# Kernel tuning notes

Hardware: AMD Instinct MI355X
Metric: run time of the kernel (lower is better)

## Reference

```python
import jax, jax.numpy as jnp
import numpy as np

N_NODES = 100000


def gcn_conv(x, W, b, src, dst, n):
    """PyG GCNConv with default add_self_loops and symmetric normalization."""
    xw = x @ W  # [N, out]
    loop = jnp.arange(n, dtype=src.dtype)
    s = jnp.concatenate([src, loop])  # source j
    d = jnp.concatenate([dst, loop])  # target i
    deg = jax.ops.segment_sum(jnp.ones_like(d, dtype=xw.dtype), d, num_segments=n)
    dinv = jnp.where(deg > 0, jax.lax.rsqrt(deg), 0.0)
    norm = dinv[s] * dinv[d]  # [E+N]
    msg = xw[s] * norm[:, None]
    out = jax.ops.segment_sum(msg, d, num_segments=n)
    return out + b


def setup_inputs() -> dict:
    key = jax.random.key(0)
    ks = jax.random.split(key, 9)
    n, e, f = N_NODES, 1600000, 512
    x = jax.random.normal(ks[0], (n, f), dtype=jnp.float32)
    edge_index = jax.random.randint(ks[1], (2, e), 0, n, dtype=jnp.int32)
    y = jax.random.uniform(ks[2], (n, 1), dtype=jnp.float32)
    W1 = jax.random.normal(ks[3], (f, 64), dtype=jnp.float32) / np.sqrt(f)
    b1 = jnp.zeros((64,), jnp.float32)
    W2 = jax.random.normal(ks[4], (64, 256), dtype=jnp.float32) / np.sqrt(64)
    b2 = jnp.zeros((256,), jnp.float32)
    W3 = jax.random.normal(ks[5], (256, 1), dtype=jnp.float32) / np.sqrt(256)
    b3 = jnp.zeros((1,), jnp.float32)
    return {"x": x, "edge_index": edge_index, "y": y,
            "W1": W1, "b1": b1, "W2": W2, "b2": b2, "W3": W3, "b3": b3}


def reference(x, edge_index, y, W1, b1, W2, b2, W3, b3):
    n = x.shape[0]
    src, dst = edge_index[0], edge_index[1]
    h = jax.nn.relu(gcn_conv(x, W1, b1, src, dst, n))
    # dropout is identity in eval mode
    h = jax.nn.relu(gcn_conv(h, W2, b2, src, dst, n))
    z = gcn_conv(h, W3, b3, src, dst, n)  # logits [N, 1]
    # BCE(sigmoid(z), y), computed stably via log-sigmoid
    loss = -(y * jax.nn.log_sigmoid(z) + (1.0 - y) * jax.nn.log_sigmoid(-z))
    return jnp.mean(loss)
```

## Files before the change

### kernel.cpp

```cpp
#include <hip/hip_runtime.h>
#include <math.h>

typedef __attribute__((ext_vector_type(8))) short s16x8;
typedef __attribute__((ext_vector_type(4))) float f32x4;

__device__ inline ushort f2bf(float f) {
    union { float f; unsigned u; } v; v.f = f;
    unsigned r = v.u + 0x7FFF + ((v.u >> 16) & 1);
    return (ushort)(r >> 16);
}
__device__ inline float bf2f(ushort h) {
    union { unsigned u; float f; } v; v.u = ((unsigned)h) << 16;
    return v.f;
}


__global__ void hist_kernel(const int* __restrict__ dst, int E, int* __restrict__ cnt) {
    int e = blockIdx.x * blockDim.x + threadIdx.x;
    if (e < E) atomicAdd(&cnt[dst[e]], 1);
}

__global__ void alloc_kernel(const int* __restrict__ cnt, int* __restrict__ row_start,
                             float* __restrict__ dinv, int* __restrict__ total, int N) {
    int i = blockIdx.x * blockDim.x + threadIdx.x;
    int lane = threadIdx.x & 63;
    int c = (i < N) ? cnt[i] : 0;
    int inc = c;
#pragma unroll
    for (int o = 1; o < 64; o <<= 1) {
        int v = __shfl_up(inc, o, 64);
        if (lane >= o) inc += v;
    }
    int wsum = __shfl(inc, 63, 64);
    int base = 0;
    if (lane == 0) base = atomicAdd(total, wsum);
    base = __shfl(base, 0, 64);
    if (i < N) {
        row_start[i] = base + inc - c;
        dinv[i] = rsqrtf((float)(c + 1));
    }
}

__global__ void scatter_kernel(const int* __restrict__ src, const int* __restrict__ dst, int E,
                               const int* __restrict__ row_start, int* __restrict__ cursor,
                               int* __restrict__ csr) {
    int e = blockIdx.x * blockDim.x + threadIdx.x;
    if (e < E) {
        int d = dst[e];
        int p = row_start[d] + atomicAdd(&cursor[d], 1);
        csr[p] = src[e];
    }
}

__global__ void wsplit_kernel(const float* __restrict__ W, ushort* __restrict__ wt_hi,
                              ushort* __restrict__ wt_lo) {
    int idx = blockIdx.x * blockDim.x + threadIdx.x;
    if (idx < 64 * 512) {
        int n = idx & 63, k = idx >> 6;
        float f = W[k * 64 + n];
        ushort h = f2bf(f);
        wt_hi[n * 512 + k] = h;
        wt_lo[n * 512 + k] = f2bf(f - bf2f(h));
    }
}

__global__ __launch_bounds__(256, 3) void gemm1_kernel(const float* __restrict__ x,
                                                       const ushort* __restrict__ wt_hi,
                                                       const ushort* __restrict__ wt_lo,
                                                       float* __restrict__ out, int N) {
    __shared__ __align__(16) short xs_hi[128 * 64];
    __shared__ __align__(16) short xs_lo[128 * 64];
    __shared__ __align__(16) short ws_hi[64 * 64];
    __shared__ __align__(16) short ws_lo[64 * 64];

    const int tid = threadIdx.x;
    const int nodeBase = blockIdx.x * 128;
    const int wave = tid >> 6, lane = tid & 63;
    const int m16 = lane & 15, quad = lane >> 4;

    f32x4 acc[2][4];
#pragma unroll
    for (int mt = 0; mt < 2; mt++)
#pragma unroll
        for (int nt = 0; nt < 4; nt++) acc[mt][nt] = (f32x4){0.f, 0.f, 0.f, 0.f};

    for (int kc = 0; kc < 512; kc += 64) {
        __syncthreads();
#pragma unroll
        for (int i = 0; i < 4; i++) {
            int f = tid + i * 256;
            int node = f >> 3, g = f & 7;
            int gn = nodeBase + node;
            if (gn >= N) gn = N - 1;
            const float4 a = *(const float4*)(x + (size_t)gn * 512 + kc + g * 8);
            const float4 b = *(const float4*)(x + (size_t)gn * 512 + kc + g * 8 + 4);
            float ff[8] = {a.x, a.y, a.z, a.w, b.x, b.y, b.z, b.w};
            union { ushort u[8]; uint4 v; } H, L;
#pragma unroll
            for (int j = 0; j < 8; j++) {
                ushort h = f2bf(ff[j]);
                H.u[j] = h;
                L.u[j] = f2bf(ff[j] - bf2f(h));
            }
            int gp = (g + node) & 7;
            *(uint4*)&xs_hi[node * 64 + gp * 8] = H.v;
            *(uint4*)&xs_lo[node * 64 + gp * 8] = L.v;
        }
#pragma unroll
        for (int i = 0; i < 2; i++) {
            int f = tid + i * 256;
            int n = f >> 3, g = f & 7;
            int gp = (g + n) & 7;
            *(uint4*)&ws_hi[n * 64 + gp * 8] =
                *(const uint4*)(wt_hi + (size_t)n * 512 + kc + g * 8);
            *(uint4*)&ws_lo[n * 64 + gp * 8] =
                *(const uint4*)(wt_lo + (size_t)n * 512 + kc + g * 8);
        }
        __syncthreads();
#pragma unroll
        for (int ck = 0; ck < 2; ck++) {
            s16x8 Ah[2], Al[2];
#pragma unroll
            for (int mt = 0; mt < 2; mt++) {
                int row = (wave * 2 + mt) * 16 + m16;
                int gp = (ck * 4 + quad + row) & 7;
                Ah[mt] = *(s16x8*)&xs_hi[row * 64 + gp * 8];
                Al[mt] = *(s16x8*)&xs_lo[row * 64 + gp * 8];
            }
#pragma unroll
            for (int nt = 0; nt < 4; nt++) {
                int n = nt * 16 + m16;
                int gp = (ck * 4 + quad + n) & 7;
                s16x8 Bh = *(s16x8*)&ws_hi[n * 64 + gp * 8];
                s16x8 Bl = *(s16x8*)&ws_lo[n * 64 + gp * 8];
#pragma unroll
                for (int mt = 0; mt < 2; mt++) {
                    acc[mt][nt] = __builtin_amdgcn_mfma_f32_16x16x32_bf16(Ah[mt], Bh, acc[mt][nt], 0, 0, 0);
                    acc[mt][nt] = __builtin_amdgcn_mfma_f32_16x16x32_bf16(Ah[mt], Bl, acc[mt][nt], 0, 0, 0);
                    acc[mt][nt] = __builtin_amdgcn_mfma_f32_16x16x32_bf16(Al[mt], Bh, acc[mt][nt], 0, 0, 0);
                }
            }
        }
    }
#pragma unroll
    for (int mt = 0; mt < 2; mt++) {
#pragma unroll
        for (int r = 0; r < 4; r++) {
            int gn = nodeBase + (wave * 2 + mt) * 16 + quad * 4 + r;
            if (gn < N) {
#pragma unroll
                for (int nt = 0; nt < 4; nt++)
                    out[(size_t)gn * 64 + nt * 16 + m16] = acc[mt][nt][r];
            }
        }
    }
}

template <int RELU, int BIAS>
__global__ void agg64_kernel(const float* __restrict__ in, float* __restrict__ out,
                             const int* __restrict__ row_start, const int* __restrict__ cnt,
                             const int* __restrict__ csr, const float* __restrict__ dinv,
                             const float* __restrict__ bias, int N) {
    int gw = (int)((blockIdx.x * (size_t)blockDim.x + threadIdx.x) >> 6);
    int lane = threadIdx.x & 63;
    if (gw >= N) return;
    float di = dinv[gw];
    float acc = di * di * in[(size_t)gw * 64 + lane];
    int s = row_start[gw];
    int c = cnt[gw];
    int e = 0;
    for (; e + 8 <= c; e += 8) {
        int j0 = csr[s + e + 0], j1 = csr[s + e + 1], j2 = csr[s + e + 2], j3 = csr[s + e + 3];
        int j4 = csr[s + e + 4], j5 = csr[s + e + 5], j6 = csr[s + e + 6], j7 = csr[s + e + 7];
        float v0 = in[(size_t)j0 * 64 + lane];
        float v1 = in[(size_t)j1 * 64 + lane];
        float v2 = in[(size_t)j2 * 64 + lane];
        float v3 = in[(size_t)j3 * 64 + lane];
        float v4 = in[(size_t)j4 * 64 + lane];
        float v5 = in[(size_t)j5 * 64 + lane];
        float v6 = in[(size_t)j6 * 64 + lane];
        float v7 = in[(size_t)j7 * 64 + lane];
        float s0 = dinv[j0] * v0 + dinv[j1] * v1 + dinv[j2] * v2 + dinv[j3] * v3;
        float s1 = dinv[j4] * v4 + dinv[j5] * v5 + dinv[j6] * v6 + dinv[j7] * v7;
        acc += di * (s0 + s1);
    }
    for (; e < c; e++) {
        int j = csr[s + e];
        acc += di * dinv[j] * in[(size_t)j * 64 + lane];
    }
    if (BIAS) acc += bias[lane];
    if (RELU) acc = fmaxf(acc, 0.f);
    out[(size_t)gw * 64 + lane] = acc;
}

__global__ __launch_bounds__(256, 2) void gemm23_kernel(const float* __restrict__ a2,
                                                        const float* __restrict__ W2,
                                                        const float* __restrict__ b2,
                                                        const float* __restrict__ W3,
                                                        float* __restrict__ t, int N) {
    __shared__ float w2s[64 * 256];
    __shared__ float b2s[256];
    __shared__ float w3s[256];
    const int tid = threadIdx.x;
#pragma unroll
    for (int i = 0; i < 16; i++) {
        int f4 = tid + i * 256;
        *(float4*)&w2s[f4 * 4] = *(const float4*)&W2[f4 * 4];
    }
    b2s[tid] = b2[tid];
    w3s[tid] = W3[tid];
    __syncthreads();

    const int lane = tid & 63;
    const int wave = tid >> 6;
    const int nodeBase = blockIdx.x * 64 + wave * 16;

    float4 w3f = *(const float4*)&w3s[lane * 4];
    float4 b2f = *(const float4*)&b2s[lane * 4];

    float acc[16][4];
#pragma unroll
    for (int n = 0; n < 16; n++) {
        acc[n][0] = 0.f; acc[n][1] = 0.f; acc[n][2] = 0.f; acc[n][3] = 0.f;
    }

    for (int k4 = 0; k4 < 64; k4 += 4) {
        float4 wf0 = *(const float4*)&w2s[(k4 + 0) * 256 + lane * 4];
        float4 wf1 = *(const float4*)&w2s[(k4 + 1) * 256 + lane * 4];
        float4 wf2 = *(const float4*)&w2s[(k4 + 2) * 256 + lane * 4];
        float4 wf3 = *(const float4*)&w2s[(k4 + 3) * 256 + lane * 4];
#pragma unroll
        for (int n = 0; n < 16; n++) {
            int gn = nodeBase + n;
            if (gn >= N) gn = N - 1;
            float4 av = *(const float4*)&a2[(size_t)gn * 64 + k4];
            acc[n][0] = fmaf(av.x, wf0.x, acc[n][0]);
            acc[n][1] = fmaf(av.x, wf0.y, acc[n][1]);
            acc[n][2] = fmaf(av.x, wf0.z, acc[n][2]);
            acc[n][3] = fmaf(av.x, wf0.w, acc[n][3]);
            acc[n][0] = fmaf(av.y, wf1.x, acc[n][0]);
            acc[n][1] = fmaf(av.y, wf1.y, acc[n][1]);
            acc[n][2] = fmaf(av.y, wf1.z, acc[n][2]);
            acc[n][3] = fmaf(av.y, wf1.w, acc[n][3]);
            acc[n][0] = fmaf(av.z, wf2.x, acc[n][0]);
            acc[n][1] = fmaf(av.z, wf2.y, acc[n][1]);
            acc[n][2] = fmaf(av.z, wf2.z, acc[n][2]);
            acc[n][3] = fmaf(av.z, wf2.w, acc[n][3]);
            acc[n][0] = fmaf(av.w, wf3.x, acc[n][0]);
            acc[n][1] = fmaf(av.w, wf3.y, acc[n][1]);
            acc[n][2] = fmaf(av.w, wf3.z, acc[n][2]);
            acc[n][3] = fmaf(av.w, wf3.w, acc[n][3]);
        }
    }

#pragma unroll
    for (int n = 0; n < 16; n++) {
        float r0 = fmaxf(acc[n][0] + b2f.x, 0.f);
        float r1 = fmaxf(acc[n][1] + b2f.y, 0.f);
        float r2 = fmaxf(acc[n][2] + b2f.z, 0.f);
        float r3 = fmaxf(acc[n][3] + b2f.w, 0.f);
        float p = r0 * w3f.x + r1 * w3f.y + r2 * w3f.z + r3 * w3f.w;
#pragma unroll
        for (int off = 32; off > 0; off >>= 1) p += __shfl_down(p, off, 64);
        int gn = nodeBase + n;
        if (lane == 0 && gn < N) t[gn] = p;
    }
}

__global__ void loss_kernel(const float* __restrict__ t, const float* __restrict__ dinv,
                            const int* __restrict__ row_start, const int* __restrict__ cnt,
                            const int* __restrict__ csr, const float* __restrict__ y,
                            const float* __restrict__ b3, float* __restrict__ out,
                            int N, float invN) {
    int i = blockIdx.x * blockDim.x + threadIdx.x;
    float loss = 0.f;
    if (i < N) {
        float di = dinv[i];
        float aedge = 0.f;
        int s = row_start[i], c = cnt[i];
        int e = 0;
        for (; e + 4 <= c; e += 4) {
            int j0 = csr[s + e + 0], j1 = csr[s + e + 1];
            int j2 = csr[s + e + 2], j3 = csr[s + e + 3];
            aedge += dinv[j0] * t[j0] + dinv[j1] * t[j1] + dinv[j2] * t[j2] + dinv[j3] * t[j3];
        }
        for (; e < c; e++) { int j = csr[s + e]; aedge += dinv[j] * t[j]; }
        float z = di * (di * t[i] + aedge) + b3[0];
        float yv = y[i];
        float L = log1pf(expf(-fabsf(z)));
        float spz  = fmaxf(z, 0.f) + L;
        float spnz = fmaxf(-z, 0.f) + L;
        loss = yv * spnz + (1.f - yv) * spz;
    }
#pragma unroll
    for (int off = 32; off > 0; off >>= 1) loss += __shfl_down(loss, off, 64);
    __shared__ float red[4];
    int lane = threadIdx.x & 63, wave = threadIdx.x >> 6;
    if (lane == 0) red[wave] = loss;
    __syncthreads();
    if (threadIdx.x == 0)
        atomicAdd(out, (red[0] + red[1] + red[2] + red[3]) * invN);
}

extern "C" void kernel_launch(void* const* d_in, const int* in_sizes, int n_in,
                              void* d_out, int out_size, void* d_ws, size_t ws_size,
                              hipStream_t stream) {
    const float* x  = (const float*)d_in[0];
    const int*   ei = (const int*)d_in[1];
    const float* y  = (const float*)d_in[2];
    const float* W1 = (const float*)d_in[3];
    const float* b1 = (const float*)d_in[4];
    const float* W2 = (const float*)d_in[5];
    const float* b2 = (const float*)d_in[6];
    const float* W3 = (const float*)d_in[7];
    const float* b3 = (const float*)d_in[8];

    const int N = in_sizes[2];
    const int E = in_sizes[1] / 2;
    const int* src  = ei;
    const int* dstp = ei + E;

    char* w = (char*)d_ws;
    int*    cnt       = (int*)w;    w += (size_t)N * 4;
    int*    cursor    = (int*)w;    w += (size_t)N * 4;
    int*    total     = (int*)w;    w += 16;
    int*    row_start = (int*)w;    w += (size_t)N * 4;
    float*  dinv      = (float*)w;  w += (size_t)N * 4;
    int*    csr       = (int*)w;    w += (size_t)E * 4;
    ushort* wt_hi     = (ushort*)w; w += (size_t)64 * 512 * 2;
    ushort* wt_lo     = (ushort*)w; w += (size_t)64 * 512 * 2;
    float*  bufA      = (float*)w;  w += (size_t)N * 64 * 4;
    float*  bufB      = (float*)w;  w += (size_t)N * 64 * 4;

    hipMemsetAsync(cnt, 0, (size_t)N * 8 + 16, stream);
    hipMemsetAsync(d_out, 0, sizeof(float), stream);

    const int tb = 256;
    wsplit_kernel<<<(64 * 512 + tb - 1) / tb, tb, 0, stream>>>(W1, wt_hi, wt_lo);
    hist_kernel<<<(E + tb - 1) / tb, tb, 0, stream>>>(dstp, E, cnt);
    alloc_kernel<<<(N + tb - 1) / tb, tb, 0, stream>>>(cnt, row_start, dinv, total, N);
    scatter_kernel<<<(E + tb - 1) / tb, tb, 0, stream>>>(src, dstp, E, row_start, cursor, csr);

    gemm1_kernel<<<(N + 127) / 128, 256, 0, stream>>>(x, wt_hi, wt_lo, bufA, N);
    agg64_kernel<1, 1><<<(N + 3) / 4, 256, 0, stream>>>(bufA, bufB, row_start, cnt, csr, dinv, b1, N);

    agg64_kernel<0, 0><<<(N + 3) / 4, 256, 0, stream>>>(bufB, bufA, row_start, cnt, csr, dinv, nullptr, N);

    gemm23_kernel<<<(N + 63) / 64, 256, 0, stream>>>(bufA, W2, b2, W3, bufB, N);

    loss_kernel<<<(N + tb - 1) / tb, tb, 0, stream>>>(bufB, dinv, row_start, cnt, csr, y, b3,
                                                      (float*)d_out, N, 1.0f / N);
}
```

Baseline: 749.2 us.

## Store intermediate features in bf16 with dinv pre-scaled into source rows

Intermediate node-feature buffers change from fp32 to bf16, which halves the bytes gathered per edge in the two aggregation passes and in the dense layer-2/3 read. The source-side dinv factor is folded into the producer (GEMM1 epilogue, first aggregation, gemm23 output), so gather loops become plain sums without per-neighbour dinv loads. This trades fp32 precision for bf16 rounding of activations, which may shift the loss slightly.

```diff
diff --git a/kernel.cpp b/kernel.cpp
--- a/kernel.cpp
+++ b/kernel.cpp
@@ -12,6 +12,12 @@
 __device__ inline float bf2f(ushort h) {
     union { unsigned u; float f; } v; v.u = ((unsigned)h) << 16;
     return v.f;
+}
+__device__ inline float bfLo(unsigned u) {
+    union { unsigned x; float f; } v; v.x = u << 16; return v.f;
+}
+__device__ inline float bfHi(unsigned u) {
+    union { unsigned x; float f; } v; v.x = u & 0xFFFF0000u; return v.f;
 }
 
 
@@ -67,7 +73,8 @@
 __global__ __launch_bounds__(256, 3) void gemm1_kernel(const float* __restrict__ x,
                                                        const ushort* __restrict__ wt_hi,
                                                        const ushort* __restrict__ wt_lo,
-                                                       float* __restrict__ out, int N) {
+                                                       const float* __restrict__ dinv,
+                                                       ushort* __restrict__ out, int N) {
     __shared__ __align__(16) short xs_hi[128 * 64];
     __shared__ __align__(16) short xs_lo[128 * 64];
     __shared__ __align__(16) short ws_hi[64 * 64];
@@ -148,56 +155,58 @@
         for (int r = 0; r < 4; r++) {
             int gn = nodeBase + (wave * 2 + mt) * 16 + quad * 4 + r;
             if (gn < N) {
+                float di = dinv[gn];
 #pragma unroll
                 for (int nt = 0; nt < 4; nt++)
-                    out[(size_t)gn * 64 + nt * 16 + m16] = acc[mt][nt][r];
+                    out[(size_t)gn * 64 + nt * 16 + m16] = f2bf(di * acc[mt][nt][r]);
             }
         }
     }
 }
 
-template <int RELU, int BIAS>
-__global__ void agg64_kernel(const float* __restrict__ in, float* __restrict__ out,
-                             const int* __restrict__ row_start, const int* __restrict__ cnt,
-                             const int* __restrict__ csr, const float* __restrict__ dinv,
-                             const float* __restrict__ bias, int N) {
+template <int RELU, int BIAS, int PREMUL>
+__global__ void agg64bf_kernel(const ushort* __restrict__ in, ushort* __restrict__ out,
+                               const int* __restrict__ row_start, const int* __restrict__ cnt,
+                               const int* __restrict__ csr, const float* __restrict__ dinv,
+                               const float* __restrict__ bias, int N) {
     int gw = (int)((blockIdx.x * (size_t)blockDim.x + threadIdx.x) >> 6);
     int lane = threadIdx.x & 63;
     if (gw >= N) return;
-    float di = dinv[gw];
-    float acc = di * di * in[(size_t)gw * 64 + lane];
+    float acc = bf2f(in[(size_t)gw * 64 + lane]);
     int s = row_start[gw];
     int c = cnt[gw];
     int e = 0;
     for (; e + 8 <= c; e += 8) {
         int j0 = csr[s + e + 0], j1 = csr[s + e + 1], j2 = csr[s + e + 2], j3 = csr[s + e + 3];
         int j4 = csr[s + e + 4], j5 = csr[s + e + 5], j6 = csr[s + e + 6], j7 = csr[s + e + 7];
-        float v0 = in[(size_t)j0 * 64 + lane];
-        float v1 = in[(size_t)j1 * 64 + lane];
-        float v2 = in[(size_t)j2 * 64 + lane];
-        float v3 = in[(size_t)j3 * 64 + lane];
-        float v4 = in[(size_t)j4 * 64 + lane];
-        float v5 = in[(size_t)j5 * 64 + lane];
-        float v6 = in[(size_t)j6 * 64 + lane];
-        float v7 = in[(size_t)j7 * 64 + lane];
-        float s0 = dinv[j0] * v0 + dinv[j1] * v1 + dinv[j2] * v2 + dinv[j3] * v3;
-        float s1 = dinv[j4] * v4 + dinv[j5] * v5 + dinv[j6] * v6 + dinv[j7] * v7;
-        acc += di * (s0 + s1);
+        float v0 = bf2f(in[(size_t)j0 * 64 + lane]);
+        float v1 = bf2f(in[(size_t)j1 * 64 + lane]);
+        float v2 = bf2f(in[(size_t)j2 * 64 + lane]);
+        float v3 = bf2f(in[(size_t)j3 * 64 + lane]);
+        float v4 = bf2f(in[(size_t)j4 * 64 + lane]);
+        float v5 = bf2f(in[(size_t)j5 * 64 + lane]);
+        float v6 = bf2f(in[(size_t)j6 * 64 + lane]);
+        float v7 = bf2f(in[(size_t)j7 * 64 + lane]);
+        acc += ((v0 + v1) + (v2 + v3)) + ((v4 + v5) + (v6 + v7));
     }
     for (; e < c; e++) {
         int j = csr[s + e];
-        acc += di * dinv[j] * in[(size_t)j * 64 + lane];
-    }
-    if (BIAS) acc += bias[lane];
-    if (RELU) acc = fmaxf(acc, 0.f);
-    out[(size_t)gw * 64 + lane] = acc;
-}
-
-__global__ __launch_bounds__(256, 2) void gemm23_kernel(const float* __restrict__ a2,
+        acc += bf2f(in[(size_t)j * 64 + lane]);
+    }
+    float di = dinv[gw];
+    float v = di * acc;
+    if (BIAS) v += bias[lane];
+    if (RELU) v = fmaxf(v, 0.f);
+    if (PREMUL) v *= di;
+    out[(size_t)gw * 64 + lane] = f2bf(v);
+}
+
+__global__ __launch_bounds__(256, 2) void gemm23_kernel(const ushort* __restrict__ a2,
                                                         const float* __restrict__ W2,
                                                         const float* __restrict__ b2,
                                                         const float* __restrict__ W3,
-                                                        float* __restrict__ t, int N) {
+                                                        const float* __restrict__ dinv,
+                                                        float* __restrict__ r, int N) {
     __shared__ float w2s[64 * 256];
     __shared__ float b2s[256];
     __shared__ float w3s[256];
@@ -233,23 +242,24 @@
         for (int n = 0; n < 16; n++) {
             int gn = nodeBase + n;
             if (gn >= N) gn = N - 1;
-            float4 av = *(const float4*)&a2[(size_t)gn * 64 + k4];
-            acc[n][0] = fmaf(av.x, wf0.x, acc[n][0]);
-            acc[n][1] = fmaf(av.x, wf0.y, acc[n][1]);
-            acc[n][2] = fmaf(av.x, wf0.z, acc[n][2]);
-            acc[n][3] = fmaf(av.x, wf0.w, acc[n][3]);
-            acc[n][0] = fmaf(av.y, wf1.x, acc[n][0]);
-            acc[n][1] = fmaf(av.y, wf1.y, acc[n][1]);
-            acc[n][2] = fmaf(av.y, wf1.z, acc[n][2]);
-            acc[n][3] = fmaf(av.y, wf1.w, acc[n][3]);
-            acc[n][0] = fmaf(av.z, wf2.x, acc[n][0]);
-            acc[n][1] = fmaf(av.z, wf2.y, acc[n][1]);
-            acc[n][2] = fmaf(av.z, wf2.z, acc[n][2]);
-            acc[n][3] = fmaf(av.z, wf2.w, acc[n][3]);
-            acc[n][0] = fmaf(av.w, wf3.x, acc[n][0]);
-            acc[n][1] = fmaf(av.w, wf3.y, acc[n][1]);
-            acc[n][2] = fmaf(av.w, wf3.z, acc[n][2]);
-            acc[n][3] = fmaf(av.w, wf3.w, acc[n][3]);
+            uint2 u = *(const uint2*)(a2 + (size_t)gn * 64 + k4);
+            float a0 = bfLo(u.x), a1 = bfHi(u.x), a2v = bfLo(u.y), a3 = bfHi(u.y);
+            acc[n][0] = fmaf(a0, wf0.x, acc[n][0]);
+            acc[n][1] = fmaf(a0, wf0.y, acc[n][1]);
+            acc[n][2] = fmaf(a0, wf0.z, acc[n][2]);
+            acc[n][3] = fmaf(a0, wf0.w, acc[n][3]);
+            acc[n][0] = fmaf(a1, wf1.x, acc[n][0]);
+            acc[n][1] = fmaf(a1, wf1.y, acc[n][1]);
+            acc[n][2] = fmaf(a1, wf1.z, acc[n][2]);
+            acc[n][3] = fmaf(a1, wf1.w, acc[n][3]);
+            acc[n][0] = fmaf(a2v, wf2.x, acc[n][0]);
+            acc[n][1] = fmaf(a2v, wf2.y, acc[n][1]);
+            acc[n][2] = fmaf(a2v, wf2.z, acc[n][2]);
+            acc[n][3] = fmaf(a2v, wf2.w, acc[n][3]);
+            acc[n][0] = fmaf(a3, wf3.x, acc[n][0]);
+            acc[n][1] = fmaf(a3, wf3.y, acc[n][1]);
+            acc[n][2] = fmaf(a3, wf3.z, acc[n][2]);
+            acc[n][3] = fmaf(a3, wf3.w, acc[n][3]);
         }
     }
 
@@ -263,11 +273,11 @@
 #pragma unroll
         for (int off = 32; off > 0; off >>= 1) p += __shfl_down(p, off, 64);
         int gn = nodeBase + n;
-        if (lane == 0 && gn < N) t[gn] = p;
-    }
-}
-
-__global__ void loss_kernel(const float* __restrict__ t, const float* __restrict__ dinv,
+        if (lane == 0 && gn < N) r[gn] = dinv[gn] * p;
+    }
+}
+
+__global__ void loss_kernel(const float* __restrict__ r, const float* __restrict__ dinv,
                             const int* __restrict__ row_start, const int* __restrict__ cnt,
                             const int* __restrict__ csr, const float* __restrict__ y,
                             const float* __restrict__ b3, float* __restrict__ out,
@@ -275,17 +285,16 @@
     int i = blockIdx.x * blockDim.x + threadIdx.x;
     float loss = 0.f;
     if (i < N) {
-        float di = dinv[i];
-        float aedge = 0.f;
+        float aedge = r[i];
         int s = row_start[i], c = cnt[i];
         int e = 0;
         for (; e + 4 <= c; e += 4) {
             int j0 = csr[s + e + 0], j1 = csr[s + e + 1];
             int j2 = csr[s + e + 2], j3 = csr[s + e + 3];
-            aedge += dinv[j0] * t[j0] + dinv[j1] * t[j1] + dinv[j2] * t[j2] + dinv[j3] * t[j3];
-        }
-        for (; e < c; e++) { int j = csr[s + e]; aedge += dinv[j] * t[j]; }
-        float z = di * (di * t[i] + aedge) + b3[0];
+            aedge += (r[j0] + r[j1]) + (r[j2] + r[j3]);
+        }
+        for (; e < c; e++) aedge += r[csr[s + e]];
+        float z = dinv[i] * aedge + b3[0];
         float yv = y[i];
         float L = log1pf(expf(-fabsf(z)));
         float spz  = fmaxf(z, 0.f) + L;
@@ -329,8 +338,9 @@
     int*    csr       = (int*)w;    w += (size_t)E * 4;
     ushort* wt_hi     = (ushort*)w; w += (size_t)64 * 512 * 2;
     ushort* wt_lo     = (ushort*)w; w += (size_t)64 * 512 * 2;
-    float*  bufA      = (float*)w;  w += (size_t)N * 64 * 4;
-    float*  bufB      = (float*)w;  w += (size_t)N * 64 * 4;
+    ushort* pbuf      = (ushort*)w; w += (size_t)N * 64 * 2;
+    ushort* qbuf      = (ushort*)w; w += (size_t)N * 64 * 2;
+    float*  rbuf      = (float*)w;  w += (size_t)N * 4;
 
     hipMemsetAsync(cnt, 0, (size_t)N * 8 + 16, stream);
     hipMemsetAsync(d_out, 0, sizeof(float), stream);
@@ -341,13 +351,12 @@
     alloc_kernel<<<(N + tb - 1) / tb, tb, 0, stream>>>(cnt, row_start, dinv, total, N);
     scatter_kernel<<<(E + tb - 1) / tb, tb, 0, stream>>>(src, dstp, E, row_start, cursor, csr);
 
-    gemm1_kernel<<<(N + 127) / 128, 256, 0, stream>>>(x, wt_hi, wt_lo, bufA, N);
-    agg64_kernel<1, 1><<<(N + 3) / 4, 256, 0, stream>>>(bufA, bufB, row_start, cnt, csr, dinv, b1, N);
-
-    agg64_kernel<0, 0><<<(N + 3) / 4, 256, 0, stream>>>(bufB, bufA, row_start, cnt, csr, dinv, nullptr, N);
-
-    gemm23_kernel<<<(N + 63) / 64, 256, 0, stream>>>(bufA, W2, b2, W3, bufB, N);
-
-    loss_kernel<<<(N + tb - 1) / tb, tb, 0, stream>>>(bufB, dinv, row_start, cnt, csr, y, b3,
+    gemm1_kernel<<<(N + 127) / 128, 256, 0, stream>>>(x, wt_hi, wt_lo, dinv, pbuf, N);
+    agg64bf_kernel<1, 1, 1><<<(N + 3) / 4, 256, 0, stream>>>(pbuf, qbuf, row_start, cnt, csr, dinv, b1, N);
+    agg64bf_kernel<0, 0, 0><<<(N + 3) / 4, 256, 0, stream>>>(qbuf, pbuf, row_start, cnt, csr, dinv, nullptr, N);
+
+    gemm23_kernel<<<(N + 63) / 64, 256, 0, stream>>>(pbuf, W2, b2, W3, dinv, rbuf, N);
+
+    loss_kernel<<<(N + tb - 1) / tb, tb, 0, stream>>>(rbuf, dinv, row_start, cnt, csr, y, b3,
                                                       (float*)d_out, N, 1.0f / N);
 }
```

Result: faster. 732.1 us (-2.3%).
